# Kernel optimization log

Measured on AMD Instinct MI355X. Metric: run time of the kernel, lower is better.

## Reference

```python
import jax, jax.numpy as jnp
import numpy as np
import math

B, N, D, H, NBT = 16, 512, 512, 8, 5
HD = D // H
EPS = 1e-5

def _ln(x, g, b):
    mu = jnp.mean(x, axis=-1, keepdims=True)
    var = jnp.mean(jnp.square(x - mu), axis=-1, keepdims=True)
    return (x - mu) * jax.lax.rsqrt(var + EPS) * g + b

def setup_inputs() -> dict:
    key = jax.random.key(0)
    ks = jax.random.split(key, 16)
    s = 0.02
    inp = {
        'x': jax.random.normal(ks[0], (B, N, D), jnp.float32),
        'adj': jax.random.randint(ks[1], (B, N, N), 0, NBT, jnp.int64),
        'mask': (jax.random.uniform(ks[2], (B, N)) > 0.1).astype(jnp.float32),
        'Wq': jax.random.normal(ks[3], (D, D), jnp.float32) * s,
        'bq': jnp.zeros((D,), jnp.float32),
        'Wk': jax.random.normal(ks[4], (D, D), jnp.float32) * s,
        'bk': jnp.zeros((D,), jnp.float32),
        'Wv': jax.random.normal(ks[5], (D, D), jnp.float32) * s,
        'bv': jnp.zeros((D,), jnp.float32),
        'Wo': jax.random.normal(ks[6], (D, D), jnp.float32) * s,
        'bo': jnp.zeros((D,), jnp.float32),
        'edge_bias': jax.random.normal(ks[7], (NBT, H), jnp.float32) * s,
        'W1': jax.random.normal(ks[8], (D, 4 * D), jnp.float32) * s,
        'b1': jnp.zeros((4 * D,), jnp.float32),
        'W2': jax.random.normal(ks[9], (4 * D, D), jnp.float32) * s,
        'b2': jnp.zeros((D,), jnp.float32),
        'g1': jnp.ones((D,), jnp.float32),
        'beta1': jnp.zeros((D,), jnp.float32),
        'g2': jnp.ones((D,), jnp.float32),
        'beta2': jnp.zeros((D,), jnp.float32),
    }
    return inp

def reference(x, adj, mask, Wq, bq, Wk, bk, Wv, bv, Wo, bo, edge_bias,
              W1, b1, W2, b2, g1, beta1, g2, beta2):
    # --- attention block ---
    residual = x
    h = _ln(x, g1, beta1)
    # (B,N,D) -> (B,H,N,HD)
    Q = (h @ Wq + bq).reshape(B, N, H, HD).transpose(0, 2, 1, 3)
    K = (h @ Wk + bk).reshape(B, N, H, HD).transpose(0, 2, 1, 3)
    V = (h @ Wv + bv).reshape(B, N, H, HD).transpose(0, 2, 1, 3)
    attn = jnp.einsum('bhqd,bhkd->bhqk', Q, K) / math.sqrt(HD)
    # per-head edge-type bias: gather (B,N,N,H) -> (B,H,N,N)
    eb = edge_bias[adj].transpose(0, 3, 1, 2)
    attn = attn + eb
    mask_2d = mask[:, None, None, :] * mask[:, None, :, None]  # (B,1,N,N)
    attn = jnp.where(mask_2d == 0, -jnp.inf, attn)
    attn = jax.nn.softmax(attn, axis=-1)
    attn = jnp.nan_to_num(attn, nan=0.0)  # fully-masked rows -> 0
    out = jnp.einsum('bhqk,bhkd->bhqd', attn, V)
    out = out.transpose(0, 2, 1, 3).reshape(B, N, D)
    out = out @ Wo + bo
    x = residual + out  # dropout is identity in eval
    # --- FFN block ---
    residual = x
    h = _ln(x, g2, beta2)
    h = jax.nn.gelu(h @ W1 + b1, approximate=False) @ W2 + b2
    x = residual + h
    return x * mask[:, :, None]
```

## Files before the change

### kernel.cpp

```cpp
#include <hip/hip_runtime.h>
#include <hip/hip_bf16.h>
#include <math.h>
#include <stdint.h>

typedef __hip_bfloat16 bf16;
typedef __bf16 bf16x8 __attribute__((ext_vector_type(8)));
typedef float f32x4 __attribute__((ext_vector_type(4)));

#define MFMA16 __builtin_amdgcn_mfma_f32_16x16x32_bf16

__device__ __forceinline__ void gll16(const void* gsrc, void* ldst) {
  __builtin_amdgcn_global_load_lds(
      (const __attribute__((address_space(1))) unsigned int*)(uintptr_t)gsrc,
      (__attribute__((address_space(3))) unsigned int*)(uintptr_t)ldst,
      16, 0, 0);
}

__global__ __launch_bounds__(256) void pack_adj(const int* __restrict__ adj,
                                                const float* __restrict__ mask,
                                                unsigned char* __restrict__ out) {
  size_t i0 = ((size_t)blockIdx.x * 256 + threadIdx.x) * 16;
  int b = (int)(i0 >> 18);
  int k0 = (int)(i0 & 511);
  const float* mb = mask + b * 512 + k0;
  const int* ap = adj + i0;
  unsigned char o16[16];
#pragma unroll
  for (int j = 0; j < 16; ++j) {
    o16[j] = (unsigned char)(ap[j] | (mb[j] == 0.f ? 0x80 : 0));
  }
  *(uint4*)(out + i0) = *(const uint4*)o16;
}

__global__ __launch_bounds__(256) void transpose_wt6(
    const float* __restrict__ s0, const float* __restrict__ s1,
    const float* __restrict__ s2, const float* __restrict__ s3,
    const float* __restrict__ s4, const float* __restrict__ s5,
    bf16* __restrict__ d0, bf16* __restrict__ d1, bf16* __restrict__ d2,
    bf16* __restrict__ d3, bf16* __restrict__ d4, bf16* __restrict__ d5) {
  __shared__ float t[32][33];
  const int bid = blockIdx.x;
  const float* W;
  bf16* Wt;
  int K, N, n0, k0;
  if (bid < 1024) {
    int mi = bid >> 8, tt = bid & 255;
    W = (mi == 0) ? s0 : (mi == 1) ? s1 : (mi == 2) ? s2 : s3;
    Wt = (mi == 0) ? d0 : (mi == 1) ? d1 : (mi == 2) ? d2 : d3;
    K = 512; N = 512; n0 = (tt & 15) * 32; k0 = (tt >> 4) * 32;
  } else if (bid < 2048) {
    int tt = bid - 1024;
    W = s4; Wt = d4; K = 512; N = 2048;
    n0 = (tt & 63) * 32; k0 = (tt >> 6) * 32;
  } else {
    int tt = bid - 2048;
    W = s5; Wt = d5; K = 2048; N = 512;
    n0 = (tt & 15) * 32; k0 = (tt >> 4) * 32;
  }
  int tx = threadIdx.x, ty = threadIdx.y;
#pragma unroll
  for (int s = 0; s < 32; s += 8) t[ty + s][tx] = W[(size_t)(k0 + ty + s) * N + n0 + tx];
  __syncthreads();
#pragma unroll
  for (int s = 0; s < 32; s += 8) Wt[(size_t)(n0 + ty + s) * K + k0 + tx] = (bf16)t[tx][ty + s];
}

__global__ __launch_bounds__(256) void ln_k(const float* __restrict__ x,
                                            const float* __restrict__ gam,
                                            const float* __restrict__ bet,
                                            bf16* __restrict__ out) {
  int l = threadIdx.x & 63, w = threadIdx.x >> 6;
  size_t row = (size_t)blockIdx.x * 4 + w;
  const float* xr = x + row * 512 + l * 8;
  float4 v0 = *(const float4*)xr;
  float4 v1 = *(const float4*)(xr + 4);
  float s = v0.x + v0.y + v0.z + v0.w + v1.x + v1.y + v1.z + v1.w;
  float q = v0.x * v0.x + v0.y * v0.y + v0.z * v0.z + v0.w * v0.w +
            v1.x * v1.x + v1.y * v1.y + v1.z * v1.z + v1.w * v1.w;
#pragma unroll
  for (int o = 1; o < 64; o <<= 1) { s += __shfl_xor(s, o); q += __shfl_xor(q, o); }
  float mean = s * (1.0f / 512.0f);
  float var = q * (1.0f / 512.0f) - mean * mean;
  float rstd = rsqrtf(var + 1e-5f);
  const float* gr = gam + l * 8;
  const float* br = bet + l * 8;
  float4 ga = *(const float4*)gr, gb = *(const float4*)(gr + 4);
  float4 ba = *(const float4*)br, bb = *(const float4*)(br + 4);
  bf16 t8[8];
  t8[0] = (bf16)((v0.x - mean) * rstd * ga.x + ba.x);
  t8[1] = (bf16)((v0.y - mean) * rstd * ga.y + ba.y);
  t8[2] = (bf16)((v0.z - mean) * rstd * ga.z + ba.z);
  t8[3] = (bf16)((v0.w - mean) * rstd * ga.w + ba.w);
  t8[4] = (bf16)((v1.x - mean) * rstd * gb.x + bb.x);
  t8[5] = (bf16)((v1.y - mean) * rstd * gb.y + bb.y);
  t8[6] = (bf16)((v1.z - mean) * rstd * gb.z + bb.z);
  t8[7] = (bf16)((v1.w - mean) * rstd * gb.w + bb.w);
  *(uint4*)(out + row * 512 + l * 8) = *(const uint4*)t8;
}

template <int MODE, int BM, int BN>
__global__ __launch_bounds__(256) void gemm_bt(
    const bf16* __restrict__ A, const bf16* __restrict__ Bt, int M, int N, int K,
    const float* __restrict__ b0, const float* __restrict__ b1p,
    const float* __restrict__ b2p, const float* __restrict__ resid,
    const float* __restrict__ mrow, float* __restrict__ outF,
    bf16* __restrict__ outH) {
  constexpr int RA = BM / 32, RB = BN / 32;
  __shared__ __align__(16) bf16 Asw[BM * 64];
  __shared__ __align__(16) bf16 Bsw[BN * 64];
  const int tid = threadIdx.x;
  const int l = tid & 63, w = tid >> 6;
  const int g = l >> 4, ln = l & 15;
  const int wm = w >> 1, wn = w & 1;
  const int m0 = blockIdx.x * BM, n0 = blockIdx.y * BN;

  f32x4 acc[RA][RB];
  f32x4 zero = {0.f, 0.f, 0.f, 0.f};
#pragma unroll
  for (int i = 0; i < RA; ++i)
#pragma unroll
    for (int j = 0; j < RB; ++j) acc[i][j] = zero;

  const bf16* aSrc[RA];
  const bf16* bSrc[RB];
#pragma unroll
  for (int rr = 0; rr < RA; ++rr) {
    int m = w * (BM / 4) + rr * 8 + (l >> 3);
    int gs = (l & 7) ^ (m & 7);
    aSrc[rr] = A + (size_t)(m0 + m) * K + gs * 8;
  }
#pragma unroll
  for (int rr = 0; rr < RB; ++rr) {
    int n = w * (BN / 4) + rr * 8 + (l >> 3);
    int gs = (l & 7) ^ (n & 7);
    bSrc[rr] = Bt + (size_t)(n0 + n) * K + gs * 8;
  }

  for (int kt = 0; kt < K; kt += 64) {
#pragma unroll
    for (int rr = 0; rr < RA; ++rr)
      gll16(aSrc[rr] + kt, &Asw[w * (BM * 16) + rr * 512]);
#pragma unroll
    for (int rr = 0; rr < RB; ++rr)
      gll16(bSrc[rr] + kt, &Bsw[w * (BN * 16) + rr * 512]);
    __syncthreads();
#pragma unroll
    for (int kk = 0; kk < 2; ++kk) {
      bf16x8 af[RA], bfr[RB];
#pragma unroll
      for (int mt = 0; mt < RA; ++mt) {
        int m = wm * (BM / 2) + mt * 16 + ln;
        af[mt] = *(const bf16x8*)&Asw[m * 64 + (((kk * 4 + g) ^ (m & 7)) * 8)];
      }
#pragma unroll
      for (int nt = 0; nt < RB; ++nt) {
        int n = wn * (BN / 2) + nt * 16 + ln;
        bfr[nt] = *(const bf16x8*)&Bsw[n * 64 + (((kk * 4 + g) ^ (n & 7)) * 8)];
      }
#pragma unroll
      for (int mt = 0; mt < RA; ++mt)
#pragma unroll
        for (int nt = 0; nt < RB; ++nt)
          acc[mt][nt] = MFMA16(af[mt], bfr[nt], acc[mt][nt], 0, 0, 0);
    }
    __syncthreads();
  }

#pragma unroll
  for (int mt = 0; mt < RA; ++mt) {
#pragma unroll
    for (int nt = 0; nt < RB; ++nt) {
#pragma unroll
      for (int r = 0; r < 4; ++r) {
        int gm = m0 + wm * (BM / 2) + mt * 16 + g * 4 + r;
        int gn = n0 + wn * (BN / 2) + nt * 16 + ln;
        float v = acc[mt][nt][r];
        if (MODE == 0) {
          int which = gn >> 9;
          int dm = gn & 511;
          const float* bb = (which == 0) ? b0 : ((which == 1) ? b1p : b2p);
          v += bb[dm];
          if (which == 0) v *= 0.125f;
          int hh = dm >> 6, hd = dm & 63;
          int bq = gm >> 9, qq = gm & 511;
          outH[(size_t)which * 4194304 + (((size_t)(bq * 8 + hh)) * 512 + qq) * 64 + hd] =
              (bf16)v;
        } else if (MODE == 1) {
          v += b0[gn] + resid[(size_t)gm * 512 + gn];
          outF[(size_t)gm * 512 + gn] = v;
        } else if (MODE == 2) {
          v += b0[gn];
          v = 0.5f * v * (1.0f + erff(v * 0.70710678118f));
          outH[(size_t)gm * 2048 + gn] = (bf16)v;
        } else {
          v += b0[gn] + resid[(size_t)gm * 512 + gn];
          v *= mrow[gm];
          outF[(size_t)gm * 512 + gn] = v;
        }
      }
    }
  }
}

__global__ __launch_bounds__(256, 4) void attn_k(
    const bf16* __restrict__ Qg, const bf16* __restrict__ Kg,
    const bf16* __restrict__ Vg, const unsigned char* __restrict__ adj8,
    const float* __restrict__ mask, const float* __restrict__ ebias,
    bf16* __restrict__ out) {
  __shared__ __align__(16) bf16 Ksw[2][64 * 64];
  __shared__ __align__(16) bf16 Vt[2][64 * 64];
  __shared__ __align__(16) bf16 Pb[4][16 * 64];
  const int tid = threadIdx.x;
  const int l = tid & 63, w = tid >> 6, g = l >> 4, ln = l & 15;
  const int bh = blockIdx.y, b = bh >> 3, h = bh & 7;
  const int qt = blockIdx.x;
  const bf16* kb = Kg + (size_t)bh * 512 * 64;
  const bf16* vb = Vg + (size_t)bh * 512 * 64;

  int ksrc_off[2];
#pragma unroll
  for (int rr = 0; rr < 2; ++rr) {
    int m = w * 16 + rr * 8 + (l >> 3);
    int gs = (l & 7) ^ (l >> 3);
    ksrc_off[rr] = m * 64 + gs * 8;
  }
  int vd0[2];
#pragma unroll
  for (int it = 0; it < 2; ++it) vd0[it] = (it * 4 + w) * 8;

  const int qrow = qt * 64 + w * 16 + ln;
  const bf16* qp = Qg + ((size_t)bh * 512 + qrow) * 64;
  bf16x8 qf0 = *(const bf16x8*)(qp + g * 8);
  bf16x8 qf1 = *(const bf16x8*)(qp + 32 + g * 8);

  const bool rowlive = mask[b * 512 + qrow] != 0.f;
  float e0 = ebias[0 * 8 + h], e1 = ebias[1 * 8 + h], e2 = ebias[2 * 8 + h];
  float e3 = ebias[3 * 8 + h], e4 = ebias[4 * 8 + h];
  const unsigned char* adjq = adj8 + ((size_t)b * 512 + qrow) * 512;

  f32x4 zero = {0.f, 0.f, 0.f, 0.f};
  f32x4 o[4];
#pragma unroll
  for (int dt = 0; dt < 4; ++dt) o[dt] = zero;
  float rsum = 0.f;
  bf16* pw = &Pb[w][0];

#pragma unroll
  for (int rr = 0; rr < 2; ++rr) gll16(kb + ksrc_off[rr], &Ksw[0][w * 1024 + rr * 512]);
#pragma unroll
  for (int it = 0; it < 2; ++it) {
    uint4 v = *(const uint4*)(vb + l * 64 + vd0[it]);
    const bf16* pv = (const bf16*)&v;
#pragma unroll
    for (int j = 0; j < 8; ++j)
      Vt[0][(vd0[it] + j) * 64 + (((l >> 3) ^ j) * 8) + (l & 7)] = pv[j];
  }
  __syncthreads();

  for (int t = 0; t < 8; ++t) {
    const int cur = t & 1, nxt = cur ^ 1;
    uint4 vv[2];
    if (t < 7) {
      const bf16* kbt = kb + (t + 1) * 4096;
#pragma unroll
      for (int rr = 0; rr < 2; ++rr)
        gll16(kbt + ksrc_off[rr], &Ksw[nxt][w * 1024 + rr * 512]);
      const bf16* vbt = vb + (t + 1) * 4096;
#pragma unroll
      for (int it = 0; it < 2; ++it) vv[it] = *(const uint4*)(vbt + l * 64 + vd0[it]);
    }

    f32x4 s[4];
#pragma unroll
    for (int t4 = 0; t4 < 4; ++t4) {
      int kr = t4 * 16 + ln;
      s[t4] = zero;
      bf16x8 a0 = *(const bf16x8*)&Ksw[cur][kr * 64 + ((g ^ (ln & 7)) * 8)];
      s[t4] = MFMA16(a0, qf0, s[t4], 0, 0, 0);
      bf16x8 a1 = *(const bf16x8*)&Ksw[cur][kr * 64 + (((4 + g) ^ (ln & 7)) * 8)];
      s[t4] = MFMA16(a1, qf1, s[t4], 0, 0, 0);
    }

    if (t < 7) {
#pragma unroll
      for (int it = 0; it < 2; ++it) {
        const bf16* pv = (const bf16*)&vv[it];
#pragma unroll
        for (int j = 0; j < 8; ++j)
          Vt[nxt][(vd0[it] + j) * 64 + (((l >> 3) ^ j) * 8) + (l & 7)] = pv[j];
      }
    }

#pragma unroll
    for (int t4 = 0; t4 < 4; ++t4) {
      int kbase = t * 64 + t4 * 16 + g * 4;
      uchar4 c4 = *(const uchar4*)(adjq + kbase);
      unsigned char cv[4] = {c4.x, c4.y, c4.z, c4.w};
      bf16 hb[4];
#pragma unroll
      for (int r = 0; r < 4; ++r) {
        int a = cv[r] & 7;
        float eb = (a == 0) ? e0 : (a == 1) ? e1 : (a == 2) ? e2 : (a == 3) ? e3 : e4;
        float p = (!rowlive || (cv[r] & 0x80)) ? 0.f : __expf(s[t4][r] + eb);
        rsum += p;
        hb[r] = (bf16)p;
      }
      int sub = t4 * 2 + (g >> 1);
      *(uint2*)&pw[ln * 64 + ((sub ^ (ln & 7)) * 8) + (g & 1) * 4] = *(const uint2*)hb;
    }

#pragma unroll
    for (int ks = 0; ks < 2; ++ks) {
      bf16x8 pa = *(const bf16x8*)&pw[ln * 64 + (((ks * 4 + g) ^ (ln & 7)) * 8)];
#pragma unroll
      for (int dt = 0; dt < 4; ++dt) {
        int d = dt * 16 + ln;
        bf16x8 vvv = *(const bf16x8*)&Vt[cur][d * 64 + (((ks * 4 + g) ^ (ln & 7)) * 8)];
        o[dt] = MFMA16(pa, vvv, o[dt], 0, 0, 0);
      }
    }
    __syncthreads();
  }

  rsum += __shfl_xor(rsum, 16);
  rsum += __shfl_xor(rsum, 32);
  float inv = (rsum > 0.f) ? 1.f / rsum : 0.f;
  const int qbase = qt * 64 + w * 16;
#pragma unroll
  for (int r = 0; r < 4; ++r) {
    float invr = __shfl(inv, g * 4 + r);
#pragma unroll
    for (int dt = 0; dt < 4; ++dt) {
      int q = qbase + g * 4 + r;
      out[((size_t)b * 512 + q) * 512 + h * 64 + dt * 16 + ln] = (bf16)(o[dt][r] * invr);
    }
  }
}

extern "C" void kernel_launch(void* const* d_in, const int* in_sizes, int n_in,
                              void* d_out, int out_size, void* d_ws, size_t ws_size,
                              hipStream_t stream) {
  const float* x = (const float*)d_in[0];
  const int* adj = (const int*)d_in[1];
  const float* mask = (const float*)d_in[2];
  const float* Wq = (const float*)d_in[3];
  const float* bq = (const float*)d_in[4];
  const float* Wk = (const float*)d_in[5];
  const float* bk = (const float*)d_in[6];
  const float* Wv = (const float*)d_in[7];
  const float* bv = (const float*)d_in[8];
  const float* Wo = (const float*)d_in[9];
  const float* bo = (const float*)d_in[10];
  const float* ebias = (const float*)d_in[11];
  const float* W1 = (const float*)d_in[12];
  const float* b1 = (const float*)d_in[13];
  const float* W2 = (const float*)d_in[14];
  const float* b2 = (const float*)d_in[15];
  const float* g1 = (const float*)d_in[16];
  const float* be1 = (const float*)d_in[17];
  const float* g2 = (const float*)d_in[18];
  const float* be2 = (const float*)d_in[19];
  float* outp = (float*)d_out;

  char* ws = (char*)d_ws;
  size_t off = 0;
  auto alloc = [&](size_t bytes) {
    void* p = ws + off;
    off += (bytes + 255) & ~(size_t)255;
    return p;
  };
  const size_t QSZ = 4194304;
  bf16* h1 = (bf16*)alloc(8192UL * 512 * 2);
  bf16* wqkv = (bf16*)alloc(1536UL * 512 * 2);
  bf16* wo_t = (bf16*)alloc(512UL * 512 * 2);
  bf16* w1_t = (bf16*)alloc(2048UL * 512 * 2);
  bf16* w2_t = (bf16*)alloc(512UL * 2048 * 2);
  bf16* qkv = (bf16*)alloc(3UL * QSZ * 2);
  bf16* aout = (bf16*)alloc(8192UL * 512 * 2);
  float* xmid = (float*)alloc(8192UL * 512 * 4);
  bf16* h2 = (bf16*)alloc(8192UL * 512 * 2);
  bf16* a1 = (bf16*)alloc(8192UL * 2048 * 2);
  unsigned char* adj8 = (unsigned char*)alloc(4194304UL);
  if (off > ws_size) return;

  pack_adj<<<1024, 256, 0, stream>>>(adj, mask, adj8);
  transpose_wt6<<<3072, dim3(32, 8), 0, stream>>>(Wq, Wk, Wv, Wo, W1, W2, wqkv,
                                                  wqkv + 512 * 512, wqkv + 1024 * 512,
                                                  wo_t, w1_t, w2_t);

  ln_k<<<2048, 256, 0, stream>>>(x, g1, be1, h1);
  gemm_bt<0, 128, 128><<<dim3(64, 12), 256, 0, stream>>>(
      h1, wqkv, 8192, 1536, 512, bq, bk, bv, nullptr, nullptr, nullptr, qkv);
  attn_k<<<dim3(8, 128), 256, 0, stream>>>(qkv, qkv + QSZ, qkv + 2 * QSZ, adj8, mask,
                                           ebias, aout);
  gemm_bt<1, 64, 64><<<dim3(128, 8), 256, 0, stream>>>(
      aout, wo_t, 8192, 512, 512, bo, nullptr, nullptr, x, nullptr, xmid, nullptr);
  ln_k<<<2048, 256, 0, stream>>>(xmid, g2, be2, h2);
  gemm_bt<2, 128, 128><<<dim3(64, 16), 256, 0, stream>>>(
      h2, w1_t, 8192, 2048, 512, b1, nullptr, nullptr, nullptr, nullptr, nullptr, a1);
  gemm_bt<3, 64, 64><<<dim3(128, 8), 256, 0, stream>>>(
      a1, w2_t, 8192, 512, 2048, b2, nullptr, nullptr, xmid, mask, outp, nullptr);
}
```

Before: 165.1 us.

## Double attention query tile per block and prefetch adjacency codes one tile ahead

The attention kernel now runs 512 threads (8 waves) per block covering 128 query rows, so each K/V tile staged in LDS is reused by twice as many queries and the grid halves. Waves 0-3 load K through global_load_lds while waves 4-7 load and transpose V, splitting the staging work by role. Adjacency bytes for the next key tile are also prefetched into registers one iteration early. The trade-off is fewer blocks (512 total), a higher launch-bounds occupancy target that may pressure registers, and more waves waiting at each barrier.

```diff
diff --git a/kernel.cpp b/kernel.cpp
--- a/kernel.cpp
+++ b/kernel.cpp
@@ -202,33 +202,35 @@
   }
 }
 
-__global__ __launch_bounds__(256, 4) void attn_k(
+__global__ __launch_bounds__(512, 6) void attn_k(
     const bf16* __restrict__ Qg, const bf16* __restrict__ Kg,
     const bf16* __restrict__ Vg, const unsigned char* __restrict__ adj8,
     const float* __restrict__ mask, const float* __restrict__ ebias,
     bf16* __restrict__ out) {
   __shared__ __align__(16) bf16 Ksw[2][64 * 64];
   __shared__ __align__(16) bf16 Vt[2][64 * 64];
-  __shared__ __align__(16) bf16 Pb[4][16 * 64];
+  __shared__ __align__(16) bf16 Pb[8][16 * 64];
   const int tid = threadIdx.x;
   const int l = tid & 63, w = tid >> 6, g = l >> 4, ln = l & 15;
+  const int sw = w & 3;
+  const bool kRole = (w < 4);
   const int bh = blockIdx.y, b = bh >> 3, h = bh & 7;
-  const int qt = blockIdx.x;
+  const int qt2 = blockIdx.x;
   const bf16* kb = Kg + (size_t)bh * 512 * 64;
   const bf16* vb = Vg + (size_t)bh * 512 * 64;
 
   int ksrc_off[2];
 #pragma unroll
   for (int rr = 0; rr < 2; ++rr) {
-    int m = w * 16 + rr * 8 + (l >> 3);
+    int m = sw * 16 + rr * 8 + (l >> 3);
     int gs = (l & 7) ^ (l >> 3);
     ksrc_off[rr] = m * 64 + gs * 8;
   }
   int vd0[2];
 #pragma unroll
-  for (int it = 0; it < 2; ++it) vd0[it] = (it * 4 + w) * 8;
-
-  const int qrow = qt * 64 + w * 16 + ln;
+  for (int it = 0; it < 2; ++it) vd0[it] = (sw * 2 + it) * 8;
+
+  const int qrow = qt2 * 128 + w * 16 + ln;
   const bf16* qp = Qg + ((size_t)bh * 512 + qrow) * 64;
   bf16x8 qf0 = *(const bf16x8*)(qp + g * 8);
   bf16x8 qf1 = *(const bf16x8*)(qp + 32 + g * 8);
@@ -245,29 +247,42 @@
   float rsum = 0.f;
   bf16* pw = &Pb[w][0];
 
-#pragma unroll
-  for (int rr = 0; rr < 2; ++rr) gll16(kb + ksrc_off[rr], &Ksw[0][w * 1024 + rr * 512]);
-#pragma unroll
-  for (int it = 0; it < 2; ++it) {
-    uint4 v = *(const uint4*)(vb + l * 64 + vd0[it]);
-    const bf16* pv = (const bf16*)&v;
-#pragma unroll
-    for (int j = 0; j < 8; ++j)
-      Vt[0][(vd0[it] + j) * 64 + (((l >> 3) ^ j) * 8) + (l & 7)] = pv[j];
-  }
+  if (kRole) {
+#pragma unroll
+    for (int rr = 0; rr < 2; ++rr) gll16(kb + ksrc_off[rr], &Ksw[0][sw * 1024 + rr * 512]);
+  } else {
+#pragma unroll
+    for (int it = 0; it < 2; ++it) {
+      uint4 v = *(const uint4*)(vb + l * 64 + vd0[it]);
+      const bf16* pv = (const bf16*)&v;
+#pragma unroll
+      for (int j = 0; j < 8; ++j)
+        Vt[0][(vd0[it] + j) * 64 + (((l >> 3) ^ j) * 8) + (l & 7)] = pv[j];
+    }
+  }
+  uchar4 c4[4];
+#pragma unroll
+  for (int t4 = 0; t4 < 4; ++t4) c4[t4] = *(const uchar4*)(adjq + t4 * 16 + g * 4);
   __syncthreads();
 
   for (int t = 0; t < 8; ++t) {
     const int cur = t & 1, nxt = cur ^ 1;
     uint4 vv[2];
+    uchar4 n4[4];
     if (t < 7) {
-      const bf16* kbt = kb + (t + 1) * 4096;
-#pragma unroll
-      for (int rr = 0; rr < 2; ++rr)
-        gll16(kbt + ksrc_off[rr], &Ksw[nxt][w * 1024 + rr * 512]);
-      const bf16* vbt = vb + (t + 1) * 4096;
-#pragma unroll
-      for (int it = 0; it < 2; ++it) vv[it] = *(const uint4*)(vbt + l * 64 + vd0[it]);
+      if (kRole) {
+        const bf16* kbt = kb + (t + 1) * 4096;
+#pragma unroll
+        for (int rr = 0; rr < 2; ++rr)
+          gll16(kbt + ksrc_off[rr], &Ksw[nxt][sw * 1024 + rr * 512]);
+      } else {
+        const bf16* vbt = vb + (t + 1) * 4096;
+#pragma unroll
+        for (int it = 0; it < 2; ++it) vv[it] = *(const uint4*)(vbt + l * 64 + vd0[it]);
+      }
+#pragma unroll
+      for (int t4 = 0; t4 < 4; ++t4)
+        n4[t4] = *(const uchar4*)(adjq + (t + 1) * 64 + t4 * 16 + g * 4);
     }
 
     f32x4 s[4];
@@ -281,7 +296,7 @@
       s[t4] = MFMA16(a1, qf1, s[t4], 0, 0, 0);
     }
 
-    if (t < 7) {
+    if (t < 7 && !kRole) {
 #pragma unroll
       for (int it = 0; it < 2; ++it) {
         const bf16* pv = (const bf16*)&vv[it];
@@ -293,9 +308,7 @@
 
 #pragma unroll
     for (int t4 = 0; t4 < 4; ++t4) {
-      int kbase = t * 64 + t4 * 16 + g * 4;
-      uchar4 c4 = *(const uchar4*)(adjq + kbase);
-      unsigned char cv[4] = {c4.x, c4.y, c4.z, c4.w};
+      unsigned char cv[4] = {c4[t4].x, c4[t4].y, c4[t4].z, c4[t4].w};
       bf16 hb[4];
 #pragma unroll
       for (int r = 0; r < 4; ++r) {
@@ -320,12 +333,16 @@
       }
     }
     __syncthreads();
+    if (t < 7) {
+#pragma unroll
+      for (int t4 = 0; t4 < 4; ++t4) c4[t4] = n4[t4];
+    }
   }
 
   rsum += __shfl_xor(rsum, 16);
   rsum += __shfl_xor(rsum, 32);
   float inv = (rsum > 0.f) ? 1.f / rsum : 0.f;
-  const int qbase = qt * 64 + w * 16;
+  const int qbase = qt2 * 128 + w * 16;
 #pragma unroll
   for (int r = 0; r < 4; ++r) {
     float invr = __shfl(inv, g * 4 + r);
@@ -391,7 +408,7 @@
   ln_k<<<2048, 256, 0, stream>>>(x, g1, be1, h1);
   gemm_bt<0, 128, 128><<<dim3(64, 12), 256, 0, stream>>>(
       h1, wqkv, 8192, 1536, 512, bq, bk, bv, nullptr, nullptr, nullptr, qkv);
-  attn_k<<<dim3(8, 128), 256, 0, stream>>>(qkv, qkv + QSZ, qkv + 2 * QSZ, adj8, mask,
+  attn_k<<<dim3(4, 128), 512, 0, stream>>>(qkv, qkv + QSZ, qkv + 2 * QSZ, adj8, mask,
                                            ebias, aout);
   gemm_bt<1, 64, 64><<<dim3(128, 8), 256, 0, stream>>>(
       aout, wo_t, 8192, 512, 512, bo, nullptr, nullptr, x, nullptr, xmid, nullptr);
```

After: 211.2 us. +27.9%, slower.
